# Kernel optimization log

Hardware: AMD Instinct MI355X
Metric: run time of the kernel (lower is better)

The kernel has to match this reference:

```python
import jax, jax.numpy as jnp
import numpy as np

K = 5          # init kwarg k: k-1 = 4 nearest neighbors used, randint over [0, k-2]
DIMS = 512     # init kwarg dims


def _pairwise_dist(X):
    # Faithful to find_k: euclidean distance matrix, computed via the
    # ||a||^2 + ||b||^2 - 2ab gram trick instead of the O(T) python loop.
    sq = jnp.sum(X * X, axis=1)
    d2 = sq[:, None] + sq[None, :] - 2.0 * (X @ X.T)
    return jnp.sqrt(jnp.maximum(d2, 0.0))


def _generate(min_samples, n_per, key):
    # SMOTE.generate: for each minority row, n_per synthetic samples, each
    # interpolated toward a uniformly chosen one of its k-1 nearest neighbors.
    T, d = min_samples.shape
    D = _pairwise_dist(min_samples)                       # [T, T]
    nbrs = jnp.argsort(D, axis=1)[:, 1:K]                 # [T, k-1], drop self
    k1, k2 = jax.random.split(key)
    choice = jax.random.randint(k1, (T, n_per), 0, K - 1)          # nn = randint(0, k-2)
    u = jax.random.uniform(k2, (T, n_per, 1), dtype=min_samples.dtype)  # uniform(0,1)
    nn_idx = jnp.take_along_axis(nbrs, choice, axis=1)    # [T, n_per]
    base = min_samples[:, None, :]                        # [T, 1, d]
    diff = min_samples[nn_idx] - base                     # [T, n_per, d]
    # populate() fills row-major (outer loop i, inner loop over N) -> reshape matches
    return (base + u * diff).reshape(T * n_per, d)


def setup_inputs() -> dict:
    key = jax.random.key(0)
    n_major, n_minor = 24576, 8192
    X = jax.random.normal(key, (n_major + n_minor, DIMS), dtype=jnp.float32)
    y = jnp.concatenate([jnp.zeros((n_major,), jnp.int32),
                         jnp.ones((n_minor,), jnp.int32)])
    return {"X": X, "y": y}


def reference(X, y):
    # forward: oversample every non-dominant class up to the dominant count.
    y_np = np.asarray(y)                       # labels are concrete constants
    occ = np.bincount(y_np)                    # == one_hot(y).sum(0)
    dom = int(occ.argmax())
    n_occ = int(occ[dom])
    key = jax.random.key(42)
    X_out = X
    y_out = y.astype(jnp.float32)
    for c in range(len(occ)):
        if c == dom:
            continue
        n_per = int((n_occ - int(occ[c])) * 100 / int(occ[c])) // 100  # int(N/100)
        if n_per <= 0:
            continue
        cand = X[y_np == c]
        key, sub = jax.random.split(key)
        xs = _generate(cand, n_per, sub)
        X_out = jnp.concatenate([X_out, xs], axis=0)
        y_out = jnp.concatenate([y_out, jnp.full((xs.shape[0],), float(c), jnp.float32)])
    return X_out, y_out
```

## Files before the change

kernel.cpp:

```cpp
#include <hip/hip_runtime.h>
#include <stdint.h>
#include <math.h>

#ifndef JAX_PARTITIONABLE
#define JAX_PARTITIONABLE 1
#endif

#define DIM    512
#define NTOT   32768
#define NMAJ   24576
#define NMIN   8192
#define NGEN   16384
#define XROWS  49152
#define Y_OFF  ((size_t)XROWS * DIM)

#define NSLICE 8
#define KSLICE 6
#define NCAND  (NSLICE * KSLICE)

#define WS_H       (NMIN)
#define WS_L       (WS_H + NMIN * DIM / 2)
#define WS_CAND_F  (WS_L + NMIN * DIM / 2)
#define WS_NBR_F   (WS_CAND_F + NMIN * NCAND / 2)

typedef __attribute__((ext_vector_type(8))) short bfv8;
typedef __attribute__((ext_vector_type(4))) float f32x4;

__device__ __forceinline__ void tf2x32(uint32_t k0, uint32_t k1,
                                       uint32_t x0, uint32_t x1,
                                       uint32_t &o0, uint32_t &o1) {
  const uint32_t ks2 = k0 ^ k1 ^ 0x1BD11BDAu;
  x0 += k0; x1 += k1;
#define TF_R(r) { x0 += x1; x1 = (x1 << (r)) | (x1 >> (32 - (r))); x1 ^= x0; }
  TF_R(13) TF_R(15) TF_R(26) TF_R(6)
  x0 += k1;  x1 += ks2 + 1u;
  TF_R(17) TF_R(29) TF_R(16) TF_R(24)
  x0 += ks2; x1 += k0 + 2u;
  TF_R(13) TF_R(15) TF_R(26) TF_R(6)
  x0 += k0;  x1 += k1 + 3u;
  TF_R(17) TF_R(29) TF_R(16) TF_R(24)
  x0 += k1;  x1 += ks2 + 4u;
  TF_R(13) TF_R(15) TF_R(26) TF_R(6)
  x0 += ks2; x1 += k0 + 5u;
#undef TF_R
  o0 = x0; o1 = x1;
}

#if JAX_PARTITIONABLE
__device__ __forceinline__ void jax_split(uint2 key, uint2 &c0, uint2 &c1) {
  tf2x32(key.x, key.y, 0u, 0u, c0.x, c0.y);
  tf2x32(key.x, key.y, 0u, 1u, c1.x, c1.y);
}
__device__ __forceinline__ uint32_t jax_bits(uint2 key, uint32_t f) {
  uint32_t a, b;
  tf2x32(key.x, key.y, 0u, f, a, b);
  return a ^ b;
}
#else
__device__ __forceinline__ void jax_split(uint2 key, uint2 &c0, uint2 &c1) {
  uint32_t a0, b0, a1, b1;
  tf2x32(key.x, key.y, 0u, 2u, a0, b0);
  tf2x32(key.x, key.y, 1u, 3u, a1, b1);
  c0 = make_uint2(a0, a1);
  c1 = make_uint2(b0, b1);
}
__device__ __forceinline__ uint32_t jax_bits(uint2 key, uint32_t f) {
  uint32_t a, b;
  if (f < (NGEN / 2)) { tf2x32(key.x, key.y, f, f + NGEN / 2, a, b); return a; }
  tf2x32(key.x, key.y, f - NGEN / 2, f, a, b); return b;
}
#endif

__device__ __forceinline__ void derive_keys(uint2 &k2, uint2 &k2i) {
  uint2 root = make_uint2(0u, 42u);
  uint2 dead, sub, k1;
  jax_split(root, dead, sub);
  jax_split(sub, k1, k2);
  jax_split(k1, dead, k2i);
}

__device__ __forceinline__ unsigned short f2bf(float x) {
  uint32_t u = __float_as_uint(x);
  uint32_t r = (u + 0x7FFFu + ((u >> 16) & 1u)) >> 16;
  return (unsigned short)r;
}

__global__ __launch_bounds__(256) void prep_kernel(const float* __restrict__ X,
                                                   float* __restrict__ wsf) {
  const int row  = blockIdx.x * 4 + (threadIdx.x >> 6);
  const int lane = threadIdx.x & 63;
  const float* Xm = X + (size_t)NMAJ * DIM;
  const float4* p = reinterpret_cast<const float4*>(Xm + (size_t)row * DIM);
  ushort4* H4 = reinterpret_cast<ushort4*>(wsf + WS_H) + (size_t)row * 128;
  double s = 0.0;
#pragma unroll
  for (int q = 0; q < 2; ++q) {
    float4 v = p[lane + q * 64];
    ushort4 h;
    h.x = f2bf(v.x); h.y = f2bf(v.y); h.z = f2bf(v.z); h.w = f2bf(v.w);
    H4[lane + q * 64] = h;
    s += (double)v.x * v.x + (double)v.y * v.y + (double)v.z * v.z + (double)v.w * v.w;
  }
#pragma unroll
  for (int off = 32; off > 0; off >>= 1) s += __shfl_down(s, off);
  if (lane == 0) wsf[row] = (float)s;
}

#define INSERT5(TD, TI, dv, jv)                                          \
  if ((dv) < TD[4]) {                                                    \
    if ((dv) < TD[3]) { TD[4]=TD[3]; TI[4]=TI[3];                        \
      if ((dv) < TD[2]) { TD[3]=TD[2]; TI[3]=TI[2];                      \
        if ((dv) < TD[1]) { TD[2]=TD[1]; TI[2]=TI[1];                    \
          if ((dv) < TD[0]) { TD[1]=TD[0]; TI[1]=TI[0]; TD[0]=(dv); TI[0]=(jv); } \
          else { TD[1]=(dv); TI[1]=(jv); } }                             \
        else { TD[2]=(dv); TI[2]=(jv); } }                               \
      else { TD[3]=(dv); TI[3]=(jv); } }                                 \
    else { TD[4]=(dv); TI[4]=(jv); } }

__global__ __launch_bounds__(256, 2) void smote_main(float* wsf) {
  __shared__ __align__(16) char raw[3 * 24576];

  const unsigned short* Hm = reinterpret_cast<const unsigned short*>(wsf + WS_H);

  const int tid = threadIdx.x;
  const int w  = tid >> 6;
  const int l  = tid & 63;
  const int wm = w & 1;
  const int wn = w >> 1;
  const int lg = l >> 4;
  const int ll = l & 15;

  const int e  = blockIdx.x >> 6;
  const int n0 = (blockIdx.x & 63) * 128;

  const int csw = (lg ^ ((ll >> 1) & 3)) * 16;
  int aoff[4], boff[4];
#pragma unroll
  for (int f = 0; f < 4; ++f) {
    aoff[f] = (wm * 64 + f * 16 + ll) * 64 + csw;
    boff[f] = 16384 + (wn * 64 + f * 16 + ll) * 64 + csw;
  }

  const int srow   = l >> 2;
  const int schunk = ((l & 3) ^ ((l >> 3) & 3)) * 16;

  auto STAGE_P = [&](int cp2, int ks2, int bi, int part) {
    char* buf = raw + bi * 24576;
    const int kb = ks2 * 64;
    const int jt = e * 1024 + cp2 * 256;
#pragma unroll
    for (int t = 0; t < 2; ++t) {
      const int idx = part * 2 + t;
      const int q = idx / 3, which = idx % 3;
      const int rb = (q * 4 + w) * 16;
      const size_t roff = (size_t)(rb + srow) * 1024 + kb + schunk;
      const char* g;
      char* dst;
      if (which == 0)      { g = (const char*)Hm + (size_t)jt * 1024 + roff;         dst = buf + rb * 64; }
      else if (which == 1) { g = (const char*)Hm + (size_t)(jt + 128) * 1024 + roff; dst = buf + 8192 + rb * 64; }
      else                 { g = (const char*)Hm + (size_t)n0 * 1024 + roff;         dst = buf + 16384 + rb * 64; }
      __builtin_amdgcn_global_load_lds(
          (const __attribute__((address_space(1))) void*)g,
          (__attribute__((address_space(3))) void*)dst, 16, 0, 0);
    }
  };

  float td[4][5];
  int   ti_[4][5];
#pragma unroll
  for (int n = 0; n < 4; ++n)
#pragma unroll
    for (int s = 0; s < 5; ++s) { td[n][s] = 1e30f; ti_[n][s] = 0x7fffffff; }

  f32x4 accA[4][4], accB[4][4];
#pragma unroll
  for (int m = 0; m < 4; ++m)
#pragma unroll
    for (int n = 0; n < 4; ++n) {
      accA[m][n] = (f32x4){0.f, 0.f, 0.f, 0.f};
      accB[m][n] = (f32x4){0.f, 0.f, 0.f, 0.f};
    }

#pragma unroll
  for (int part = 0; part < 3; ++part) STAGE_P(0, 0, 0, part);
#pragma unroll
  for (int part = 0; part < 3; ++part) STAGE_P(0, 1, 1, part);

  int cur = 0;
  int ks = 0, cp = 0;
  int pks = 2, pcp = 0, pb = 2;

  for (int s = 0; s < 64; ++s) {
    asm volatile("s_waitcnt vmcnt(6)" ::: "memory");
    __builtin_amdgcn_s_barrier();
    __builtin_amdgcn_sched_barrier(0);

    const char* buf = raw + cur * 24576;
    bfv8 bf[4], afA[4], afB[4];

#pragma unroll
    for (int n = 0; n < 4; ++n) bf[n] = *reinterpret_cast<const bfv8*>(buf + boff[n]);
    afA[0] = *reinterpret_cast<const bfv8*>(buf + aoff[0]);
    afA[1] = *reinterpret_cast<const bfv8*>(buf + aoff[1]);

    afA[2] = *reinterpret_cast<const bfv8*>(buf + aoff[2]);
    afA[3] = *reinterpret_cast<const bfv8*>(buf + aoff[3]);
    STAGE_P(pcp, pks, pb, 0);
    asm volatile("s_waitcnt lgkmcnt(2)" ::: "memory");
    __builtin_amdgcn_sched_barrier(0);
    __builtin_amdgcn_s_setprio(1);
#pragma unroll
    for (int m = 0; m < 2; ++m)
#pragma unroll
      for (int n = 0; n < 4; ++n)
        accA[m][n] = __builtin_amdgcn_mfma_f32_16x16x32_bf16(afA[m], bf[n], accA[m][n], 0, 0, 0);
    __builtin_amdgcn_s_setprio(0);
    __builtin_amdgcn_s_barrier();

    afB[0] = *reinterpret_cast<const bfv8*>(buf + 8192 + aoff[0]);
    afB[1] = *reinterpret_cast<const bfv8*>(buf + 8192 + aoff[1]);
    STAGE_P(pcp, pks, pb, 1);
    asm volatile("s_waitcnt lgkmcnt(2)" ::: "memory");
    __builtin_amdgcn_sched_barrier(0);
    __builtin_amdgcn_s_setprio(1);
#pragma unroll
    for (int m = 2; m < 4; ++m)
#pragma unroll
      for (int n = 0; n < 4; ++n)
        accA[m][n] = __builtin_amdgcn_mfma_f32_16x16x32_bf16(afA[m], bf[n], accA[m][n], 0, 0, 0);
    __builtin_amdgcn_s_setprio(0);
    __builtin_amdgcn_s_barrier();

    afB[2] = *reinterpret_cast<const bfv8*>(buf + 8192 + aoff[2]);
    afB[3] = *reinterpret_cast<const bfv8*>(buf + 8192 + aoff[3]);
    STAGE_P(pcp, pks, pb, 2);
    asm volatile("s_waitcnt lgkmcnt(2)" ::: "memory");
    __builtin_amdgcn_sched_barrier(0);
    __builtin_amdgcn_s_setprio(1);
#pragma unroll
    for (int m = 0; m < 2; ++m)
#pragma unroll
      for (int n = 0; n < 4; ++n)
        accB[m][n] = __builtin_amdgcn_mfma_f32_16x16x32_bf16(afB[m], bf[n], accB[m][n], 0, 0, 0);
    __builtin_amdgcn_s_setprio(0);
    __builtin_amdgcn_s_barrier();

    asm volatile("s_waitcnt lgkmcnt(0)" ::: "memory");
    __builtin_amdgcn_sched_barrier(0);
    __builtin_amdgcn_s_setprio(1);
#pragma unroll
    for (int m = 2; m < 4; ++m)
#pragma unroll
      for (int n = 0; n < 4; ++n)
        accB[m][n] = __builtin_amdgcn_mfma_f32_16x16x32_bf16(afB[m], bf[n], accB[m][n], 0, 0, 0);
    __builtin_amdgcn_s_setprio(0);

    if (++pks == 16) { pks = 0; ++pcp; if (pcp == 4) pcp = 0; }
    if (++pb == 3) pb = 0;

    if (ks == 15) {
      const int jt = e * 1024 + cp * 256;
#pragma unroll
      for (int m = 0; m < 4; ++m) {
        const int jb = jt + wm * 64 + m * 16 + lg * 4;
        const float4 mj = *reinterpret_cast<const float4*>(&wsf[jb]);
        const float mjr[4] = {mj.x, mj.y, mj.z, mj.w};
#pragma unroll
        for (int r = 0; r < 4; ++r) {
#pragma unroll
          for (int n = 0; n < 4; ++n) {
            const float mv = mjr[r] - 2.0f * accA[m][n][r];
            INSERT5(td[n], ti_[n], mv, jb + r);
          }
        }
      }
#pragma unroll
      for (int m = 0; m < 4; ++m) {
        const int jb = jt + 128 + wm * 64 + m * 16 + lg * 4;
        const float4 mj = *reinterpret_cast<const float4*>(&wsf[jb]);
        const float mjr[4] = {mj.x, mj.y, mj.z, mj.w};
#pragma unroll
        for (int r = 0; r < 4; ++r) {
#pragma unroll
          for (int n = 0; n < 4; ++n) {
            const float mv = mjr[r] - 2.0f * accB[m][n][r];
            INSERT5(td[n], ti_[n], mv, jb + r);
          }
        }
      }
#pragma unroll
      for (int m = 0; m < 4; ++m)
#pragma unroll
        for (int n = 0; n < 4; ++n) {
          accA[m][n] = (f32x4){0.f, 0.f, 0.f, 0.f};
          accB[m][n] = (f32x4){0.f, 0.f, 0.f, 0.f};
        }
    }
    if (++ks == 16) { ks = 0; ++cp; }
    if (++cur == 3) cur = 0;
  }

  asm volatile("s_waitcnt vmcnt(0)" ::: "memory");
  __syncthreads();

  float* md = reinterpret_cast<float*>(raw);
  int*   mi = reinterpret_cast<int*>(raw + 20480);
  const int lid = wm * 4 + lg;
#pragma unroll
  for (int n = 0; n < 4; ++n) {
    const int col = wn * 64 + n * 16 + ll;
#pragma unroll
    for (int s = 0; s < 5; ++s) {
      md[(lid * 5 + s) * 128 + col] = td[n][s];
      mi[(lid * 5 + s) * 128 + col] = ti_[n][s];
    }
  }
  __syncthreads();
  if (tid < 128) {
    unsigned short* cand = reinterpret_cast<unsigned short*>(wsf + WS_CAND_F)
                         + (size_t)(n0 + tid) * NCAND + e * KSLICE;
    float ld = -1e31f; int li = -1;
    for (int s = 0; s < KSLICE; ++s) {
      float bd = 1e30f; int bi = 0x7fffffff;
      for (int c = 0; c < 40; ++c) {
        const float d = md[c * 128 + tid];
        const int  ix = mi[c * 128 + tid];
        const bool gt_last = (d > ld) || (d == ld && ix > li);
        const bool lt_best = (d < bd) || (d == bd && ix < bi);
        if (gt_last && lt_best) { bd = d; bi = ix; }
      }
      ld = bd; li = bi;
      cand[s] = (unsigned short)bi;
    }
  }
}

__global__ __launch_bounds__(256) void rerank_kernel(const float* __restrict__ X,
                                                     float* __restrict__ wsf) {
  __shared__ unsigned long long keys_s[4][NCAND];
  const float* Xm = X + (size_t)NMAJ * DIM;
  const int wave = threadIdx.x >> 6;
  const int lane = threadIdx.x & 63;
  const int row  = blockIdx.x * 4 + wave;

  const unsigned short* cand = reinterpret_cast<const unsigned short*>(wsf + WS_CAND_F)
                             + (size_t)row * NCAND;
  const float si = wsf[row];
  const float4* Xi = reinterpret_cast<const float4*>(Xm + (size_t)row * DIM);
  const float4 xi0 = Xi[lane], xi1 = Xi[lane + 64];

  const int jv = (lane < NCAND) ? (int)cand[lane] : 0;

#pragma unroll 4
  for (int c = 0; c < NCAND; ++c) {
    const int j = __shfl(jv, c);
    const float4* Xj = reinterpret_cast<const float4*>(Xm + (size_t)j * DIM);
    const float4 xj0 = Xj[lane], xj1 = Xj[lane + 64];
    double s = (double)xi0.x * xj0.x + (double)xi0.y * xj0.y
             + (double)xi0.z * xj0.z + (double)xi0.w * xj0.w
             + (double)xi1.x * xj1.x + (double)xi1.y * xj1.y
             + (double)xi1.z * xj1.z + (double)xi1.w * xj1.w;
#pragma unroll
    for (int off = 32; off > 0; off >>= 1) s += __shfl_down(s, off);
    if (lane == 0) {
      const float d2 = (si + wsf[j]) - 2.0f * (float)s;
      const float d  = (float)sqrt((double)fmaxf(d2, 0.0f));
      keys_s[wave][c] = ((unsigned long long)__float_as_uint(d) << 32) | (uint32_t)j;
    }
  }

  unsigned long long key = (lane < NCAND) ? keys_s[wave][lane] : ~0ull;
  int* nbr = reinterpret_cast<int*>(wsf) + WS_NBR_F + (size_t)row * 4;
#pragma unroll
  for (int s = 0; s < 5; ++s) {
    unsigned long long k = key;
#pragma unroll
    for (int off = 32; off > 0; off >>= 1) {
      const unsigned long long o = __shfl_xor(k, off);
      if (o < k) k = o;
    }
    if (key == k) key = ~0ull;
    if (s >= 1 && lane == 0) nbr[s - 1] = (int)(k & 0xffffffffu);
  }
}

__global__ __launch_bounds__(256) void gen_kernel(const float* __restrict__ X,
                                                  const float* __restrict__ wsf,
                                                  float* __restrict__ out) {
  __shared__ int   nbr_s[32][4];
  __shared__ float u_s[64];
  __shared__ int   nb_s[64];
  const float* Xm = X + (size_t)NMAJ * DIM;
  const int r0 = blockIdx.x * 32;
  const int tid = threadIdx.x;

  if (tid < 32) {
    const int* nb = reinterpret_cast<const int*>(wsf) + WS_NBR_F + (size_t)(r0 + tid) * 4;
#pragma unroll
    for (int s = 0; s < 4; ++s) nbr_s[tid][s] = nb[s];
  }
  __syncthreads();
  if (tid < 64) {
    uint2 k2, k2i;
    derive_keys(k2, k2i);
    const uint32_t f = (uint32_t)(2 * r0 + tid);
    const uint32_t ch = jax_bits(k2i, f) & 3u;
    nb_s[tid] = nbr_s[tid >> 1][ch];
    const uint32_t ub = jax_bits(k2, f);
    u_s[tid] = __uint_as_float((ub >> 9) | 0x3f800000u) - 1.0f;
  }
  __syncthreads();

  const int c = tid * 2;
  for (int g = 0; g < 64; ++g) {
    const int i = g >> 1;
    const float u = u_s[g];
    const int nb = nb_s[g];
    float2 bv = *reinterpret_cast<const float2*>(Xm + (size_t)(r0 + i) * DIM + c);
    float2 nv = *reinterpret_cast<const float2*>(Xm + (size_t)nb * DIM + c);
    float2 o;
    o.x = bv.x + u * (nv.x - bv.x);
    o.y = bv.y + u * (nv.y - bv.y);
    *reinterpret_cast<float2*>(out + ((size_t)(NTOT + 2 * r0 + g)) * DIM + c) = o;
  }
}

__global__ __launch_bounds__(256) void copy_kernel(const float* __restrict__ X,
                                                   const int* __restrict__ y,
                                                   float* __restrict__ out) {
  const long long XF4 = (long long)NTOT * DIM / 4;
  const long long YF4 = XROWS / 4;
  long long idx = (long long)blockIdx.x * blockDim.x + threadIdx.x;
  const long long stride = (long long)gridDim.x * blockDim.x;
  for (long long i = idx; i < XF4 + YF4; i += stride) {
    if (i < XF4) {
      reinterpret_cast<float4*>(out)[i] = reinterpret_cast<const float4*>(X)[i];
    } else {
      long long j = i - XF4;
      float4 o;
      if (j < NTOT / 4) {
        int4 yv = reinterpret_cast<const int4*>(y)[j];
        o.x = (float)yv.x; o.y = (float)yv.y; o.z = (float)yv.z; o.w = (float)yv.w;
      } else {
        o.x = o.y = o.z = o.w = 1.0f;
      }
      reinterpret_cast<float4*>(out + Y_OFF)[j] = o;
    }
  }
}

extern "C" void kernel_launch(void* const* d_in, const int* in_sizes, int n_in,
                              void* d_out, int out_size, void* d_ws, size_t ws_size,
                              hipStream_t stream) {
  const float* X = (const float*)d_in[0];
  const int*   y = (const int*)d_in[1];
  float* out = (float*)d_out;
  float* wsf = (float*)d_ws;
  (void)in_sizes; (void)n_in; (void)out_size; (void)ws_size;

  prep_kernel  <<<dim3(NMIN / 4),  dim3(256), 0, stream>>>(X, wsf);
  smote_main   <<<dim3(512),       dim3(256), 0, stream>>>(wsf);
  rerank_kernel<<<dim3(NMIN / 4),  dim3(256), 0, stream>>>(X, wsf);
  gen_kernel   <<<dim3(NMIN / 32), dim3(256), 0, stream>>>(X, wsf, out);
  copy_kernel  <<<dim3(2048),      dim3(256), 0, stream>>>(X, y, out);
}
```

Measured before the change: 252.3 us.

## Simplify GEMM pipeline, branchless top-5 insert, merge gen and copy kernels

The main distance GEMM loop drops its fine-grained interleaving of staged async loads, partial LDS reads and MFMA groups with intermediate barriers. It now issues all staging at the top of each step, loads all fragments, then runs all MFMAs. The top-5 insertion becomes a wave-uniform early-out (__any) followed by branchless selects, to reduce divergence. The gen and copy kernels merge into one launch so the generation and the bulk copy can overlap, at the risk of losing the latency hiding the old interleaved schedule gave.

After: 243.5 us. 1.04x faster.

```diff
diff --git a/kernel.cpp b/kernel.cpp
--- a/kernel.cpp
+++ b/kernel.cpp
@@ -106,16 +106,22 @@
   if (lane == 0) wsf[row] = (float)s;
 }
 
-#define INSERT5(TD, TI, dv, jv)                                          \
-  if ((dv) < TD[4]) {                                                    \
-    if ((dv) < TD[3]) { TD[4]=TD[3]; TI[4]=TI[3];                        \
-      if ((dv) < TD[2]) { TD[3]=TD[2]; TI[3]=TI[2];                      \
-        if ((dv) < TD[1]) { TD[2]=TD[1]; TI[2]=TI[1];                    \
-          if ((dv) < TD[0]) { TD[1]=TD[0]; TI[1]=TI[0]; TD[0]=(dv); TI[0]=(jv); } \
-          else { TD[1]=(dv); TI[1]=(jv); } }                             \
-        else { TD[2]=(dv); TI[2]=(jv); } }                               \
-      else { TD[3]=(dv); TI[3]=(jv); } }                                 \
-    else { TD[4]=(dv); TI[4]=(jv); } }
+#define INSERT5B(TD, TI, dv, jv)                                           \
+  { const bool b4 = (dv) < TD[4];                                          \
+    if (__any(b4)) {                                                       \
+      const bool b3 = (dv) < TD[3], b2 = (dv) < TD[2];                     \
+      const bool b1 = (dv) < TD[1], b0 = (dv) < TD[0];                     \
+      TD[4] = b3 ? TD[3] : (b4 ? (dv) : TD[4]);                            \
+      TI[4] = b3 ? TI[3] : (b4 ? (jv) : TI[4]);                            \
+      TD[3] = b2 ? TD[2] : (b3 ? (dv) : TD[3]);                            \
+      TI[3] = b2 ? TI[2] : (b3 ? (jv) : TI[3]);                            \
+      TD[2] = b1 ? TD[1] : (b2 ? (dv) : TD[2]);                            \
+      TI[2] = b1 ? TI[1] : (b2 ? (jv) : TI[2]);                            \
+      TD[1] = b0 ? TD[0] : (b1 ? (dv) : TD[1]);                            \
+      TI[1] = b0 ? TI[0] : (b1 ? (jv) : TI[1]);                            \
+      TD[0] = b0 ? (dv) : TD[0];                                           \
+      TI[0] = b0 ? (jv) : TI[0];                                           \
+    } }
 
 __global__ __launch_bounds__(256, 2) void smote_main(float* wsf) {
   __shared__ __align__(16) char raw[3 * 24576];
@@ -144,24 +150,26 @@
   const int srow   = l >> 2;
   const int schunk = ((l & 3) ^ ((l >> 3) & 3)) * 16;
 
-  auto STAGE_P = [&](int cp2, int ks2, int bi, int part) {
+  auto STAGE = [&](int cp2, int ks2, int bi) {
     char* buf = raw + bi * 24576;
     const int kb = ks2 * 64;
     const int jt = e * 1024 + cp2 * 256;
 #pragma unroll
-    for (int t = 0; t < 2; ++t) {
-      const int idx = part * 2 + t;
-      const int q = idx / 3, which = idx % 3;
+    for (int q = 0; q < 2; ++q) {
       const int rb = (q * 4 + w) * 16;
       const size_t roff = (size_t)(rb + srow) * 1024 + kb + schunk;
-      const char* g;
-      char* dst;
-      if (which == 0)      { g = (const char*)Hm + (size_t)jt * 1024 + roff;         dst = buf + rb * 64; }
-      else if (which == 1) { g = (const char*)Hm + (size_t)(jt + 128) * 1024 + roff; dst = buf + 8192 + rb * 64; }
-      else                 { g = (const char*)Hm + (size_t)n0 * 1024 + roff;         dst = buf + 16384 + rb * 64; }
+      const char* ga0 = (const char*)Hm + (size_t)jt * 1024 + roff;
+      const char* ga1 = (const char*)Hm + (size_t)(jt + 128) * 1024 + roff;
+      const char* gb  = (const char*)Hm + (size_t)n0 * 1024 + roff;
       __builtin_amdgcn_global_load_lds(
-          (const __attribute__((address_space(1))) void*)g,
-          (__attribute__((address_space(3))) void*)dst, 16, 0, 0);
+          (const __attribute__((address_space(1))) void*)ga0,
+          (__attribute__((address_space(3))) void*)(buf + rb * 64), 16, 0, 0);
+      __builtin_amdgcn_global_load_lds(
+          (const __attribute__((address_space(1))) void*)ga1,
+          (__attribute__((address_space(3))) void*)(buf + 8192 + rb * 64), 16, 0, 0);
+      __builtin_amdgcn_global_load_lds(
+          (const __attribute__((address_space(1))) void*)gb,
+          (__attribute__((address_space(3))) void*)(buf + 16384 + rb * 64), 16, 0, 0);
     }
   };
 
@@ -181,10 +189,8 @@
       accB[m][n] = (f32x4){0.f, 0.f, 0.f, 0.f};
     }
 
-#pragma unroll
-  for (int part = 0; part < 3; ++part) STAGE_P(0, 0, 0, part);
-#pragma unroll
-  for (int part = 0; part < 3; ++part) STAGE_P(0, 1, 1, part);
+  STAGE(0, 0, 0);
+  STAGE(0, 1, 1);
 
   int cur = 0;
   int ks = 0, cp = 0;
@@ -195,68 +201,31 @@
     __builtin_amdgcn_s_barrier();
     __builtin_amdgcn_sched_barrier(0);
 
+    STAGE(pcp, pks, pb);
+    if (++pks == 16) { pks = 0; ++pcp; if (pcp == 4) pcp = 0; }
+    if (++pb == 3) pb = 0;
+
     const char* buf = raw + cur * 24576;
     bfv8 bf[4], afA[4], afB[4];
-
-#pragma unroll
-    for (int n = 0; n < 4; ++n) bf[n] = *reinterpret_cast<const bfv8*>(buf + boff[n]);
-    afA[0] = *reinterpret_cast<const bfv8*>(buf + aoff[0]);
-    afA[1] = *reinterpret_cast<const bfv8*>(buf + aoff[1]);
-
-    afA[2] = *reinterpret_cast<const bfv8*>(buf + aoff[2]);
-    afA[3] = *reinterpret_cast<const bfv8*>(buf + aoff[3]);
-    STAGE_P(pcp, pks, pb, 0);
-    asm volatile("s_waitcnt lgkmcnt(2)" ::: "memory");
-    __builtin_amdgcn_sched_barrier(0);
+#pragma unroll
+    for (int n = 0; n < 4; ++n) bf[n]  = *reinterpret_cast<const bfv8*>(buf + boff[n]);
+#pragma unroll
+    for (int m = 0; m < 4; ++m) afA[m] = *reinterpret_cast<const bfv8*>(buf + aoff[m]);
+#pragma unroll
+    for (int m = 0; m < 4; ++m) afB[m] = *reinterpret_cast<const bfv8*>(buf + 8192 + aoff[m]);
+
     __builtin_amdgcn_s_setprio(1);
 #pragma unroll
-    for (int m = 0; m < 2; ++m)
+    for (int m = 0; m < 4; ++m)
 #pragma unroll
       for (int n = 0; n < 4; ++n)
         accA[m][n] = __builtin_amdgcn_mfma_f32_16x16x32_bf16(afA[m], bf[n], accA[m][n], 0, 0, 0);
-    __builtin_amdgcn_s_setprio(0);
-    __builtin_amdgcn_s_barrier();
-
-    afB[0] = *reinterpret_cast<const bfv8*>(buf + 8192 + aoff[0]);
-    afB[1] = *reinterpret_cast<const bfv8*>(buf + 8192 + aoff[1]);
-    STAGE_P(pcp, pks, pb, 1);
-    asm volatile("s_waitcnt lgkmcnt(2)" ::: "memory");
-    __builtin_amdgcn_sched_barrier(0);
-    __builtin_amdgcn_s_setprio(1);
-#pragma unroll
-    for (int m = 2; m < 4; ++m)
-#pragma unroll
-      for (int n = 0; n < 4; ++n)
-        accA[m][n] = __builtin_amdgcn_mfma_f32_16x16x32_bf16(afA[m], bf[n], accA[m][n], 0, 0, 0);
-    __builtin_amdgcn_s_setprio(0);
-    __builtin_amdgcn_s_barrier();
-
-    afB[2] = *reinterpret_cast<const bfv8*>(buf + 8192 + aoff[2]);
-    afB[3] = *reinterpret_cast<const bfv8*>(buf + 8192 + aoff[3]);
-    STAGE_P(pcp, pks, pb, 2);
-    asm volatile("s_waitcnt lgkmcnt(2)" ::: "memory");
-    __builtin_amdgcn_sched_barrier(0);
-    __builtin_amdgcn_s_setprio(1);
-#pragma unroll
-    for (int m = 0; m < 2; ++m)
+#pragma unroll
+    for (int m = 0; m < 4; ++m)
 #pragma unroll
       for (int n = 0; n < 4; ++n)
         accB[m][n] = __builtin_amdgcn_mfma_f32_16x16x32_bf16(afB[m], bf[n], accB[m][n], 0, 0, 0);
     __builtin_amdgcn_s_setprio(0);
-    __builtin_amdgcn_s_barrier();
-
-    asm volatile("s_waitcnt lgkmcnt(0)" ::: "memory");
-    __builtin_amdgcn_sched_barrier(0);
-    __builtin_amdgcn_s_setprio(1);
-#pragma unroll
-    for (int m = 2; m < 4; ++m)
-#pragma unroll
-      for (int n = 0; n < 4; ++n)
-        accB[m][n] = __builtin_amdgcn_mfma_f32_16x16x32_bf16(afB[m], bf[n], accB[m][n], 0, 0, 0);
-    __builtin_amdgcn_s_setprio(0);
-
-    if (++pks == 16) { pks = 0; ++pcp; if (pcp == 4) pcp = 0; }
-    if (++pb == 3) pb = 0;
 
     if (ks == 15) {
       const int jt = e * 1024 + cp * 256;
@@ -270,7 +239,7 @@
 #pragma unroll
           for (int n = 0; n < 4; ++n) {
             const float mv = mjr[r] - 2.0f * accA[m][n][r];
-            INSERT5(td[n], ti_[n], mv, jb + r);
+            INSERT5B(td[n], ti_[n], mv, jb + r);
           }
         }
       }
@@ -284,7 +253,7 @@
 #pragma unroll
           for (int n = 0; n < 4; ++n) {
             const float mv = mjr[r] - 2.0f * accB[m][n][r];
-            INSERT5(td[n], ti_[n], mv, jb + r);
+            INSERT5B(td[n], ti_[n], mv, jb + r);
           }
         }
       }
@@ -384,67 +353,66 @@
   }
 }
 
-__global__ __launch_bounds__(256) void gen_kernel(const float* __restrict__ X,
-                                                  const float* __restrict__ wsf,
-                                                  float* __restrict__ out) {
-  __shared__ int   nbr_s[32][4];
-  __shared__ float u_s[64];
-  __shared__ int   nb_s[64];
+__global__ __launch_bounds__(256) void emit_kernel(const float* __restrict__ X,
+                                                   const int* __restrict__ y,
+                                                   const float* __restrict__ wsf,
+                                                   float* __restrict__ out) {
   const float* Xm = X + (size_t)NMAJ * DIM;
-  const int r0 = blockIdx.x * 32;
+  const int bid = blockIdx.x;
   const int tid = threadIdx.x;
 
-  if (tid < 32) {
-    const int* nb = reinterpret_cast<const int*>(wsf) + WS_NBR_F + (size_t)(r0 + tid) * 4;
-#pragma unroll
-    for (int s = 0; s < 4; ++s) nbr_s[tid][s] = nb[s];
-  }
-  __syncthreads();
-  if (tid < 64) {
-    uint2 k2, k2i;
-    derive_keys(k2, k2i);
-    const uint32_t f = (uint32_t)(2 * r0 + tid);
-    const uint32_t ch = jax_bits(k2i, f) & 3u;
-    nb_s[tid] = nbr_s[tid >> 1][ch];
-    const uint32_t ub = jax_bits(k2, f);
-    u_s[tid] = __uint_as_float((ub >> 9) | 0x3f800000u) - 1.0f;
-  }
-  __syncthreads();
-
-  const int c = tid * 2;
-  for (int g = 0; g < 64; ++g) {
-    const int i = g >> 1;
-    const float u = u_s[g];
-    const int nb = nb_s[g];
-    float2 bv = *reinterpret_cast<const float2*>(Xm + (size_t)(r0 + i) * DIM + c);
-    float2 nv = *reinterpret_cast<const float2*>(Xm + (size_t)nb * DIM + c);
-    float2 o;
-    o.x = bv.x + u * (nv.x - bv.x);
-    o.y = bv.y + u * (nv.y - bv.y);
-    *reinterpret_cast<float2*>(out + ((size_t)(NTOT + 2 * r0 + g)) * DIM + c) = o;
-  }
-}
-
-__global__ __launch_bounds__(256) void copy_kernel(const float* __restrict__ X,
-                                                   const int* __restrict__ y,
-                                                   float* __restrict__ out) {
-  const long long XF4 = (long long)NTOT * DIM / 4;
-  const long long YF4 = XROWS / 4;
-  long long idx = (long long)blockIdx.x * blockDim.x + threadIdx.x;
-  const long long stride = (long long)gridDim.x * blockDim.x;
-  for (long long i = idx; i < XF4 + YF4; i += stride) {
-    if (i < XF4) {
-      reinterpret_cast<float4*>(out)[i] = reinterpret_cast<const float4*>(X)[i];
-    } else {
-      long long j = i - XF4;
-      float4 o;
-      if (j < NTOT / 4) {
-        int4 yv = reinterpret_cast<const int4*>(y)[j];
-        o.x = (float)yv.x; o.y = (float)yv.y; o.z = (float)yv.z; o.w = (float)yv.w;
+  if (bid < 256) {
+    __shared__ int   nbr_s[32][4];
+    __shared__ float u_s[64];
+    __shared__ int   nb_s[64];
+    const int r0 = bid * 32;
+    if (tid < 32) {
+      const int* nb = reinterpret_cast<const int*>(wsf) + WS_NBR_F + (size_t)(r0 + tid) * 4;
+#pragma unroll
+      for (int s = 0; s < 4; ++s) nbr_s[tid][s] = nb[s];
+    }
+    __syncthreads();
+    if (tid < 64) {
+      uint2 k2, k2i;
+      derive_keys(k2, k2i);
+      const uint32_t f = (uint32_t)(2 * r0 + tid);
+      const uint32_t ch = jax_bits(k2i, f) & 3u;
+      nb_s[tid] = nbr_s[tid >> 1][ch];
+      const uint32_t ub = jax_bits(k2, f);
+      u_s[tid] = __uint_as_float((ub >> 9) | 0x3f800000u) - 1.0f;
+    }
+    __syncthreads();
+    const int c = tid * 2;
+    for (int g = 0; g < 64; ++g) {
+      const int i = g >> 1;
+      const float u = u_s[g];
+      const int nb = nb_s[g];
+      float2 bv = *reinterpret_cast<const float2*>(Xm + (size_t)(r0 + i) * DIM + c);
+      float2 nv = *reinterpret_cast<const float2*>(Xm + (size_t)nb * DIM + c);
+      float2 o;
+      o.x = bv.x + u * (nv.x - bv.x);
+      o.y = bv.y + u * (nv.y - bv.y);
+      *reinterpret_cast<float2*>(out + ((size_t)(NTOT + 2 * r0 + g)) * DIM + c) = o;
+    }
+  } else {
+    const long long XF4 = (long long)NTOT * DIM / 4;
+    const long long YF4 = XROWS / 4;
+    long long idx = (long long)(bid - 256) * 256 + tid;
+    const long long stride = (long long)(gridDim.x - 256) * 256;
+    for (long long i = idx; i < XF4 + YF4; i += stride) {
+      if (i < XF4) {
+        reinterpret_cast<float4*>(out)[i] = reinterpret_cast<const float4*>(X)[i];
       } else {
-        o.x = o.y = o.z = o.w = 1.0f;
+        long long j = i - XF4;
+        float4 o;
+        if (j < NTOT / 4) {
+          int4 yv = reinterpret_cast<const int4*>(y)[j];
+          o.x = (float)yv.x; o.y = (float)yv.y; o.z = (float)yv.z; o.w = (float)yv.w;
+        } else {
+          o.x = o.y = o.z = o.w = 1.0f;
+        }
+        reinterpret_cast<float4*>(out + Y_OFF)[j] = o;
       }
-      reinterpret_cast<float4*>(out + Y_OFF)[j] = o;
     }
   }
 }
@@ -458,9 +426,8 @@
   float* wsf = (float*)d_ws;
   (void)in_sizes; (void)n_in; (void)out_size; (void)ws_size;
 
-  prep_kernel  <<<dim3(NMIN / 4),  dim3(256), 0, stream>>>(X, wsf);
-  smote_main   <<<dim3(512),       dim3(256), 0, stream>>>(wsf);
-  rerank_kernel<<<dim3(NMIN / 4),  dim3(256), 0, stream>>>(X, wsf);
-  gen_kernel   <<<dim3(NMIN / 32), dim3(256), 0, stream>>>(X, wsf, out);
-  copy_kernel  <<<dim3(2048),      dim3(256), 0, stream>>>(X, y, out);
-}
+  prep_kernel  <<<dim3(NMIN / 4), dim3(256), 0, stream>>>(X, wsf);
+  smote_main   <<<dim3(512),      dim3(256), 0, stream>>>(wsf);
+  rerank_kernel<<<dim3(NMIN / 4), dim3(256), 0, stream>>>(X, wsf);
+  emit_kernel  <<<dim3(2304),     dim3(256), 0, stream>>>(X, y, wsf, out);
+}
```
